# Optimization experiments

Measured on AMD Instinct MI355X. Metric: run time of the kernel, lower is better.

Reference implementation:

```python
import jax, jax.numpy as jnp
import numpy as np

SEQ_LEN, BATCH, INPUT, HID, LAYERS, TARGET_LEN = 120, 2048, 6, 64, 4, 120


def _cell(x_t, h, c, Wih, Whh, b):
    # torch LSTM gate order: input, forget, cell(g), output
    gates = x_t @ Wih.T + h @ Whh.T + b  # [B, 4H]
    i, f, g, o = jnp.split(gates, 4, axis=-1)
    c_new = jax.nn.sigmoid(f) * c + jax.nn.sigmoid(i) * jnp.tanh(g)
    h_new = jax.nn.sigmoid(o) * jnp.tanh(c_new)
    return h_new, c_new


def _stack_step(h, c, x_t, Wih0, Wih, Whh, b):
    # one time step through all stacked layers; h, c: [L, B, H]
    hs, cs = [], []
    inp = x_t
    L = Whh.shape[0]
    for l in range(L):
        W = Wih0 if l == 0 else Wih[l - 1]
        hn, cn = _cell(inp, h[l], c[l], W, Whh[l], b[l])
        hs.append(hn)
        cs.append(cn)
        inp = hn
    return jnp.stack(hs), jnp.stack(cs), inp


def setup_inputs() -> dict:
    key = jax.random.key(0)
    ks = jax.random.split(key, 11)
    s = 1.0 / np.sqrt(HID)  # torch LSTM uniform init scale
    u = lambda k, shp: jax.random.uniform(k, shp, jnp.float32, -s, s)
    return {
        "x": jax.random.normal(ks[0], (SEQ_LEN, BATCH, INPUT), jnp.float32),
        "enc_Wih0": u(ks[1], (4 * HID, INPUT)),
        "enc_Wih": u(ks[2], (LAYERS - 1, 4 * HID, HID)),
        "enc_Whh": u(ks[3], (LAYERS, 4 * HID, HID)),
        "enc_b": u(ks[4], (LAYERS, 4 * HID)),
        "dec_Wih0": u(ks[5], (4 * HID, INPUT)),
        "dec_Wih": u(ks[6], (LAYERS - 1, 4 * HID, HID)),
        "dec_Whh": u(ks[7], (LAYERS, 4 * HID, HID)),
        "dec_b": u(ks[8], (LAYERS, 4 * HID)),
        "lin_W": u(ks[9], (INPUT, HID)),
        "lin_b": u(ks[10], (INPUT,)),
        "target_len": TARGET_LEN,
    }


def reference(x, enc_Wih0, enc_Wih, enc_Whh, enc_b,
              dec_Wih0, dec_Wih, dec_Whh, dec_b, lin_W, lin_b, target_len):
    L, B, H = enc_Whh.shape[0], x.shape[1], enc_Whh.shape[-1]
    h0 = jnp.zeros((L, B, H), x.dtype)

    # ---- encoder: stacked LSTM over the input sequence (zero init state) ----
    def enc_step(carry, x_t):
        h, c = carry
        h, c, _ = _stack_step(h, c, x_t, enc_Wih0, enc_Wih, enc_Whh, enc_b)
        return (h, c), None

    (h, c), _ = jax.lax.scan(enc_step, (h0, h0), x)

    # ---- decoder: recursive one-step decode for target_len steps ----
    def dec_step(carry, _):
        h, c, inp = carry
        h, c, top = _stack_step(h, c, inp, dec_Wih0, dec_Wih, dec_Whh, dec_b)
        out = top @ lin_W.T + lin_b  # [B, INPUT]
        return (h, c, out), out

    last_in = x[-1]  # decoder seeded with last observed frame
    _, outputs = jax.lax.scan(dec_step, (h, c, last_in), None, length=target_len)
    return outputs  # [target_len, B, INPUT]
```

## Files before the change

kernel.cpp:

```cpp
#include <hip/hip_runtime.h>


#define S_LEN 120
#define BATCH 2048
#define NIN   6
#define H     64
#define NL    4
#define TLEN  120

#define HPAD 72

#define FRAGS_HALF 60
#define PACK_H8    (2 * FRAGS_HALF * 4 * 64)
#define PROJ_H8    (2 * 64)
#define NPACK      ((PACK_H8 + PROJ_H8) * 8)
#define EPACK_EL   (256 * 64 * 8)
#define NTOT       (NPACK + EPACK_EL)

#define WS_HOFF (768 * 1024)
#define WS_COFF (WS_HOFF + 1024 * 1024)

#define PERM(kk) ((((kk) & 3) << 4) | ((kk) >> 2))
#define PI(c)    ((((c) & 15) << 2) | ((c) >> 4))

#define SNEG (-1.44269504088896341f)
#define SGG  ( 2.88539008177792681f)
#define GGCLAMP 57.7078016355585362f
#define C2L2E 2.88539008177792681f

typedef _Float16 h8    __attribute__((ext_vector_type(8)));
typedef _Float16 hh2   __attribute__((ext_vector_type(2)));
typedef float    f32x4 __attribute__((ext_vector_type(4)));

__device__ __forceinline__ void bar_lgkm() {
  asm volatile("s_waitcnt lgkmcnt(0)\n\ts_barrier" ::: "memory");
}

__device__ __forceinline__ float swz16(float v) {
  int i = __builtin_bit_cast(int, v);
  i = __builtin_amdgcn_ds_swizzle(i, 0x401F);
  return __builtin_bit_cast(float, i);
}

__device__ __forceinline__ float ex2(float x) {
#if __has_builtin(__builtin_amdgcn_exp2f)
  return __builtin_amdgcn_exp2f(x);
#else
  return __expf(x * 0.693147180559945309f);
#endif
}

__global__ void prep_weights(const float* __restrict__ eWih0,
                             const float* __restrict__ eWih,
                             const float* __restrict__ eWhh,
                             const float* __restrict__ dWih0,
                             const float* __restrict__ dWih,
                             const float* __restrict__ dWhh,
                             const float* __restrict__ linW,
                             _Float16* __restrict__ wq) {
  int idx = blockIdx.x * blockDim.x + threadIdx.x;
  if (idx >= NTOT) return;

  if (idx >= NPACK) {
    int p    = idx - NPACK;
    int j    = p & 7;
    int lane = (p >> 3) & 63;
    int fe   = p >> 9;
    int kt   = fe & 3, nt = (fe >> 2) & 15, l = fe >> 6;
    int g    = nt * 16 + (lane & 15);
    int koff = ((lane >> 4) << 3) + j;
    float v = 0.0f;
    if (l == 0) {
      if (kt == 0)      v = (koff < NIN) ? eWih0[g * NIN + koff] : 0.0f;
      else if (kt == 1) v = 0.0f;
      else { int kk = (kt - 2) * 32 + koff; v = eWhh[g * H + PERM(kk)]; }
    } else {
      if (kt < 2) { int kk = kt * 32 + koff;
                    v = eWih[((l - 1) * 256 + g) * H + PERM(kk)]; }
      else        { int kk = (kt - 2) * 32 + koff;
                    v = eWhh[(l * 256 + g) * H + PERM(kk)]; }
    }
    v *= ((nt >> 2) == 2) ? SGG : SNEG;
    wq[idx] = (_Float16)v;
    return;
  }

  if (idx >= PACK_H8 * 8) {
    int p    = idx - PACK_H8 * 8;
    int j    = p & 7;
    int lane = (p >> 3) & 63;
    int fr   = p >> 9;
    int m    = lane & 15;
    int k    = fr * 32 + ((lane >> 4) << 3) + j;
    wq[idx] = (_Float16)((m < NIN) ? linW[m * H + k] : 0.0f);
    return;
  }

  const int j    = idx & 7;
  const int lane = (idx >> 3) & 63;
  const int wv   = (idx >> 9) & 3;
  const int fh   = idx >> 11;
  const int f    = fh % FRAGS_HALF;
  const int half = fh / FRAGS_HALF;
  const float* Wi0 = half ? dWih0 : eWih0;
  const float* Wi  = half ? dWih  : eWih;
  const float* Wh  = half ? dWhh  : eWhh;
  int l, q, kt;
  if (f < 12) { l = 0; q = f / 3; kt = f % 3; }
  else        { int ff = f - 12; l = 1 + ff / 16; ff %= 16; q = ff / 4; kt = ff % 4; }
  const int g    = q * 64 + wv * 16 + (lane & 15);
  const int k_in = ((lane >> 4) << 3) + j;
  float v;
  if (l == 0) {
    if (kt == 0) v = (k_in < NIN) ? Wi0[g * NIN + k_in] : 0.0f;
    else         v = Wh[g * H + (kt - 1) * 32 + k_in];
  } else {
    if (kt < 2) v = Wi[((l - 1) * 256 + g) * H + kt * 32 + k_in];
    else        v = Wh[(l * 256 + g) * H + (kt - 2) * 32 + k_in];
  }
  v *= (q == 2) ? SGG : SNEG;
  wq[idx] = (_Float16)v;
}

__device__ __forceinline__ float rcpf(float x) { return __builtin_amdgcn_rcpf(x); }
__device__ __forceinline__ f32x4 mf(h8 a, h8 b, f32x4 c) {
  return __builtin_amdgcn_mfma_f32_16x16x32_f16(a, b, c, 0, 0, 0);
}
#define SPLAT(v) ((f32x4){(v), (v), (v), (v)})

__device__ __forceinline__ float ew_one(float gi, float gf, float gg, float go,
                                        float& c) {
  gg = fminf(fmaxf(gg, -GGCLAMP), GGCLAMP);
  float eni = ex2(gi);
  float e2g = ex2(gg);
  float enf = ex2(gf);
  float eno = ex2(go);
  c = c * rcpf(1.0f + enf) + (e2g - 1.0f) * rcpf((1.0f + eni) * (e2g + 1.0f));
  float cc = fminf(fmaxf(c, -20.0f), 20.0f);
  float e2c = ex2(cc * C2L2E);
  return (e2c - 1.0f) * rcpf((1.0f + eno) * (e2c + 1.0f));
}

__device__ __forceinline__ void cell_ew(f32x4 g0, f32x4 g1, f32x4 g2, f32x4 g3,
                                        f32x4& c, _Float16* outbuf,
                                        int quad, int r16, int sl) {
  #pragma unroll
  for (int r = 0; r < 4; r++) {
    float cv = c[r];
    float hv = ew_one(g0[r], g1[r], g2[r], g3[r], cv);
    c[r] = cv;
    outbuf[(quad * 4 + r) * HPAD + sl * 16 + r16] = (_Float16)hv;
  }
}

__device__ __forceinline__ void precc(const h8 (&w)[8], h8 ar0, h8 ar1,
                                      f32x4 b, f32x4 (&ac)[4]) {
  #pragma unroll
  for (int q = 0; q < 4; q++)
    ac[q] = mf(ar1, w[q * 2 + 1], mf(ar0, w[q * 2], SPLAT(b[q])));
}
__device__ __forceinline__ void fireHc(const h8 (&w)[8], h8 ai0, h8 ai1,
                                       const f32x4 (&ac)[4], f32x4& c,
                                       _Float16* outbuf, int quad, int r16, int sl) {
  f32x4 g0 = mf(ai1, w[1], mf(ai0, w[0], ac[0]));
  f32x4 g1 = mf(ai1, w[3], mf(ai0, w[2], ac[1]));
  f32x4 g2 = mf(ai1, w[5], mf(ai0, w[4], ac[2]));
  f32x4 g3 = mf(ai1, w[7], mf(ai0, w[6], ac[3]));
  cell_ew(g0, g1, g2, g3, c, outbuf, quad, r16, sl);
}
__device__ __forceinline__ void fire0c(const h8 (&w)[4], h8 ax,
                                       const f32x4 (&ac)[4], f32x4& c,
                                       _Float16* outbuf, int quad, int r16, int sl) {
  f32x4 g0 = mf(ax, w[0], ac[0]);
  f32x4 g1 = mf(ax, w[1], ac[1]);
  f32x4 g2 = mf(ax, w[2], ac[2]);
  f32x4 g3 = mf(ax, w[3], ac[3]);
  cell_ew(g0, g1, g2, g3, c, outbuf, quad, r16, sl);
}
__device__ __forceinline__ void readA(const _Float16* buf, int r16, int quad,
                                      h8& a0, h8& a1) {
  a0 = *(const h8*)(buf + r16 * HPAD + quad * 8);
  a1 = *(const h8*)(buf + r16 * HPAD + 32 + quad * 8);
}

__global__ void __launch_bounds__(512, 2)
lstm_enc(const float* __restrict__ X,
         const float* __restrict__ encb,
         const h8* __restrict__ WQ,
         _Float16* __restrict__ hG,
         float* __restrict__ cG) {
  __shared__ _Float16 Hb[NL][2][16][HPAD];
  __shared__ _Float16 Xb[2][16][HPAD];

  const int tid  = threadIdx.x;
  const int wv   = tid >> 6;
  const int lane = tid & 63;
  const int quad = lane >> 4;
  const int r16  = lane & 15;
  const int grp  = wv & 1;
  const int lw   = (wv >> 1) & 3;
  const int bbase = blockIdx.x * 16;

  {
    float* p = (float*)&Hb[0][0][0][0];
    for (int i = tid; i < 4608; i += 512) p[i] = 0.0f;
    float* px = (float*)&Xb[0][0][0];
    for (int i = tid; i < 1152; i += 512) px[i] = 0.0f;
  }
  if (tid < 16 * NIN) {
    int m = tid / NIN, ii = tid - m * NIN;
    Xb[0][m][ii] = (_Float16)X[((size_t)0 * BATCH + bbase + m) * NIN + ii];
  }

  h8 we[8][4];
  #pragma unroll
  for (int q = 0; q < 4; q++)
    #pragma unroll
    for (int cc = 0; cc < 2; cc++)
      #pragma unroll
      for (int kt = 0; kt < 4; kt++)
        we[q * 2 + cc][kt] =
            WQ[(PACK_H8 + PROJ_H8) +
               ((lw * 64 + (q * 4 + 2 * grp + cc) * 4 + kt) * 64 + lane)];
  float ben[8];
  #pragma unroll
  for (int q = 0; q < 4; q++)
    #pragma unroll
    for (int cc = 0; cc < 2; cc++)
      ben[q * 2 + cc] = encb[lw * 256 + q * 64 + (2 * grp + cc) * 16 + r16] *
                        ((q == 2) ? SGG : SNEG);

  f32x4 ce[2];
  ce[0] = SPLAT(0.f); ce[1] = SPLAT(0.f);

  const bool pfLane = (wv == 0) && (lane < 48);
  const int  pe0 = lane * 2, pe1 = pe0 + 1;
  const int  pm0 = pe0 / NIN, pc0 = pe0 % NIN;
  const int  pm1 = pe1 / NIN, pc1 = pe1 % NIN;
  float pf0 = 0.f, pf1 = 0.f;
  if (pfLane) {
    const float* xs = X + ((size_t)1 * BATCH + bbase) * NIN;
    pf0 = xs[pe0]; pf1 = xs[pe1];
  }

  __syncthreads();

  #pragma unroll 1
  for (int i = 0; i < S_LEN + NL - 1; i++) {
    const int p = i & 1;
    const bool active = (i >= lw) && (i - lw < S_LEN);
    if (active) {
      const _Float16* inb = (lw == 0) ? &Xb[p][0][0] : &Hb[lw - 1][p ^ 1][0][0];
      const _Float16* rcb = &Hb[lw][p ^ 1][0][0];
      h8 ai0 = *(const h8*)(inb + r16 * HPAD + quad * 8);
      h8 ai1 = {};
      if (lw) ai1 = *(const h8*)(inb + r16 * HPAD + 32 + quad * 8);
      h8 ar0 = *(const h8*)(rcb + r16 * HPAD + quad * 8);
      h8 ar1 = *(const h8*)(rcb + r16 * HPAD + 32 + quad * 8);

      float nf0 = 0.f, nf1 = 0.f;
      if (pfLane && (i + 2 < S_LEN)) {
        const float* xs = X + ((size_t)(i + 2) * BATCH + bbase) * NIN;
        nf0 = xs[pe0]; nf1 = xs[pe1];
      }

      f32x4 a[8];
      #pragma unroll
      for (int j = 0; j < 8; j++) {
        f32x4 t = SPLAT(ben[j]);
        t = mf(ai0, we[j][0], t);
        if (lw) t = mf(ai1, we[j][1], t);
        t = mf(ar0, we[j][2], t);
        t = mf(ar1, we[j][3], t);
        a[j] = t;
      }

      _Float16* wb = &Hb[lw][p][0][0];
      #pragma unroll
      for (int r = 0; r < 4; r++) {
        hh2 hv;
        #pragma unroll
        for (int cc = 0; cc < 2; cc++) {
          float cv = ce[cc][r];
          hv[cc] = (_Float16)ew_one(a[cc][r], a[2 + cc][r],
                                    a[4 + cc][r], a[6 + cc][r], cv);
          ce[cc][r] = cv;
        }
        *(hh2*)(wb + (quad * 4 + r) * HPAD + 4 * r16 + 2 * grp) = hv;
      }

      if (pfLane && (i + 1 < S_LEN)) {
        Xb[p ^ 1][pm0][pc0] = (_Float16)pf0;
        Xb[p ^ 1][pm1][pc1] = (_Float16)pf1;
      }
      pf0 = nf0; pf1 = nf1;
    }
    bar_lgkm();
  }

  #pragma unroll
  for (int cc = 0; cc < 2; cc++)
    #pragma unroll
    for (int r = 0; r < 4; r++)
      cG[((size_t)lw * BATCH + bbase + quad * 4 + r) * H +
         (2 * grp + cc) * 16 + r16] = ce[cc][r];

  #pragma unroll
  for (int u = 0; u < 8; u++) {
    int i2 = tid + u * 512;
    int c = i2 & 63, m = (i2 >> 6) & 15, l = (i2 >> 10) & 3;
    hG[((size_t)l * BATCH + bbase + m) * H + c] =
        Hb[l][(l + 1) & 1][m][PI(c)];
  }
}

__global__ void __launch_bounds__(512, 2)
lstm_dec(const float* __restrict__ X,
         const float* __restrict__ decb,
         const float* __restrict__ linb,
         const h8* __restrict__ WQ,
         const _Float16* __restrict__ hG,
         const float* __restrict__ cG,
         float* __restrict__ out) {
  __shared__ _Float16 Hb[NL][2][16][HPAD];
  __shared__ f32x4 ACs[NL][4][4][64];

  const int tid   = threadIdx.x;
  const int wv    = tid >> 6;
  const int sl    = wv & 3;
  const int roleP = wv >> 2;
  const int lane  = tid & 63;
  const int quad  = lane >> 4;
  const int r16   = lane & 15;
  const int bbase = blockIdx.x * 16;

  #pragma unroll
  for (int u = 0; u < 8; u++) {
    int i2 = tid + u * 512;
    int l = i2 >> 10, m = (i2 >> 6) & 15, c = i2 & 63;
    Hb[l][1][m][c] = hG[((size_t)l * BATCH + bbase + m) * H + c];
  }
  __syncthreads();

  if (roleP) {
    h8 wp0[8], wpH[3][8];
    #pragma unroll
    for (int e = 0; e < 8; e++) {
      int q = e >> 1, k = e & 1;
      wp0[e] = WQ[((FRAGS_HALF + q * 3 + 1 + k) * 4 + sl) * 64 + lane];
    }
    #pragma unroll
    for (int l = 0; l < 3; l++)
      #pragma unroll
      for (int e = 0; e < 8; e++) {
        int q = e >> 1, k = e & 1;
        wpH[l][e] = WQ[((FRAGS_HALF + 12 + l * 16 + q * 4 + 2 + k) * 4 + sl) * 64 + lane];
      }
    f32x4 b0, b1, b2, b3;
    #pragma unroll
    for (int q = 0; q < 4; q++) {
      const float s = (q == 2) ? SGG : SNEG;
      b0[q] = decb[0 * 256 + q * 64 + sl * 16 + r16] * s;
      b1[q] = decb[1 * 256 + q * 64 + sl * 16 + r16] * s;
      b2[q] = decb[2 * 256 + q * 64 + sl * 16 + r16] * s;
      b3[q] = decb[3 * 256 + q * 64 + sl * 16 + r16] * s;
    }

    {
      h8 s0, s1;
      f32x4 a[4];
      readA(&Hb[0][1][0][0], r16, quad, s0, s1);
      precc(wp0, s0, s1, b0, a);
      #pragma unroll
      for (int j = 0; j < 4; j++) ACs[0][sl][j][lane] = a[j];
      readA(&Hb[1][1][0][0], r16, quad, s0, s1);
      precc(wpH[0], s0, s1, b1, a);
      #pragma unroll
      for (int j = 0; j < 4; j++) ACs[1][sl][j][lane] = a[j];
      readA(&Hb[2][1][0][0], r16, quad, s0, s1);
      precc(wpH[1], s0, s1, b2, a);
      #pragma unroll
      for (int j = 0; j < 4; j++) ACs[2][sl][j][lane] = a[j];
    }
    bar_lgkm();

    #pragma unroll 1
    for (int t = 0; t < TLEN; t++) {
      const int cur = t & 1, prv = cur ^ 1;
      {
        h8 a0, a1; readA(&Hb[3][prv][0][0], r16, quad, a0, a1);
        f32x4 a[4]; precc(wpH[2], a0, a1, b3, a);
        #pragma unroll
        for (int j = 0; j < 4; j++) ACs[3][sl][j][lane] = a[j];
        bar_lgkm();
      }
      {
        h8 a0, a1; readA(&Hb[0][cur][0][0], r16, quad, a0, a1);
        f32x4 a[4]; precc(wp0, a0, a1, b0, a);
        #pragma unroll
        for (int j = 0; j < 4; j++) ACs[0][sl][j][lane] = a[j];
        bar_lgkm();
      }
      {
        h8 a0, a1; readA(&Hb[1][cur][0][0], r16, quad, a0, a1);
        f32x4 a[4]; precc(wpH[0], a0, a1, b1, a);
        #pragma unroll
        for (int j = 0; j < 4; j++) ACs[1][sl][j][lane] = a[j];
        bar_lgkm();
      }
      {
        h8 a0, a1; readA(&Hb[2][cur][0][0], r16, quad, a0, a1);
        f32x4 a[4]; precc(wpH[1], a0, a1, b2, a);
        #pragma unroll
        for (int j = 0; j < 4; j++) ACs[2][sl][j][lane] = a[j];
        bar_lgkm();
      }
    }
  } else {
    h8 wf0[4], wfH[3][8];
    #pragma unroll
    for (int q = 0; q < 4; q++)
      wf0[q] = WQ[((FRAGS_HALF + q * 3) * 4 + sl) * 64 + lane];
    #pragma unroll
    for (int l = 0; l < 3; l++)
      #pragma unroll
      for (int e = 0; e < 8; e++) {
        int q = e >> 1, k = e & 1;
        wfH[l][e] = WQ[((FRAGS_HALF + 12 + l * 16 + q * 4 + k) * 4 + sl) * 64 + lane];
      }

    f32x4 cs0, cs1, cs2, cs3;
    #pragma unroll
    for (int r = 0; r < 4; r++) {
      cs0[r] = cG[((size_t)0 * BATCH + bbase + quad * 4 + r) * H + sl * 16 + r16];
      cs1[r] = cG[((size_t)1 * BATCH + bbase + quad * 4 + r) * H + sl * 16 + r16];
      cs2[r] = cG[((size_t)2 * BATCH + bbase + quad * 4 + r) * H + sl * 16 + r16];
      cs3[r] = cG[((size_t)3 * BATCH + bbase + quad * 4 + r) * H + sl * 16 + r16];
    }

    h8 lwA0 = WQ[PACK_H8 + lane];
    h8 lwA1 = WQ[PACK_H8 + 64 + lane];
    f32x4 lbq;
    #pragma unroll
    for (int r = 0; r < 4; r++)
      lbq[r] = (quad * 4 + r < NIN) ? linb[quad * 4 + r] : 0.0f;

    h8 xseed = {};
    if (quad == 0) {
      const float* xs = X + ((size_t)(S_LEN - 1) * BATCH + bbase + r16) * NIN;
      #pragma unroll
      for (int j = 0; j < 6; j++) xseed[j] = (_Float16)xs[j];
    }

    bar_lgkm();

    __builtin_amdgcn_s_setprio(1);

    #pragma unroll 1
    for (int t = 0; t < TLEN; t++) {
      const int cur = t & 1, prv = cur ^ 1;
      {
        h8 ar0, ar1;
        readA(&Hb[3][prv][0][0], r16, quad, ar0, ar1);
        h8 ax;
        if (t == 0) {
          ax = xseed;
        } else {
          f32x4 ap = lbq;
          ap = mf(lwA0, ar0, ap);
          ap = mf(lwA1, ar1, ap);
          if (sl == 0) {
            #pragma unroll
            for (int r = 0; r < 4; r++) {
              const int fm = quad * 4 + r;
              if (fm < NIN)
                out[((size_t)(t - 1) * BATCH + bbase + r16) * NIN + fm] = ap[r];
            }
          }
          float x4 = swz16(ap[0]);
          float x5 = swz16(ap[1]);
          h8 xa = {};
          xa[0] = (_Float16)ap[0]; xa[1] = (_Float16)ap[1];
          xa[2] = (_Float16)ap[2]; xa[3] = (_Float16)ap[3];
          xa[4] = (_Float16)x4;    xa[5] = (_Float16)x5;
          h8 zz = {};
          ax = (quad == 0) ? xa : zz;
        }
        f32x4 ac[4];
        #pragma unroll
        for (int j = 0; j < 4; j++) ac[j] = ACs[0][sl][j][lane];
        fire0c(wf0, ax, ac, cs0, &Hb[0][cur][0][0], quad, r16, sl);
        bar_lgkm();
      }
      {
        h8 ai0, ai1;
        readA(&Hb[0][cur][0][0], r16, quad, ai0, ai1);
        f32x4 ac[4];
        #pragma unroll
        for (int j = 0; j < 4; j++) ac[j] = ACs[1][sl][j][lane];
        fireHc(wfH[0], ai0, ai1, ac, cs1, &Hb[1][cur][0][0], quad, r16, sl);
        bar_lgkm();
      }
      {
        h8 ai0, ai1;
        readA(&Hb[1][cur][0][0], r16, quad, ai0, ai1);
        f32x4 ac[4];
        #pragma unroll
        for (int j = 0; j < 4; j++) ac[j] = ACs[2][sl][j][lane];
        fireHc(wfH[1], ai0, ai1, ac, cs2, &Hb[2][cur][0][0], quad, r16, sl);
        bar_lgkm();
      }
      {
        h8 ai0, ai1;
        readA(&Hb[2][cur][0][0], r16, quad, ai0, ai1);
        f32x4 ac[4];
        #pragma unroll
        for (int j = 0; j < 4; j++) ac[j] = ACs[3][sl][j][lane];
        fireHc(wfH[2], ai0, ai1, ac, cs3, &Hb[3][cur][0][0], quad, r16, sl);
        bar_lgkm();
      }
    }

    __builtin_amdgcn_s_setprio(0);

    if (sl == 0) {
      h8 ar0, ar1;
      readA(&Hb[3][1][0][0], r16, quad, ar0, ar1);
      f32x4 ap = lbq;
      ap = mf(lwA0, ar0, ap);
      ap = mf(lwA1, ar1, ap);
      #pragma unroll
      for (int r = 0; r < 4; r++) {
        const int fm = quad * 4 + r;
        if (fm < NIN)
          out[((size_t)(TLEN - 1) * BATCH + bbase + r16) * NIN + fm] = ap[r];
      }
    }
  }
}

extern "C" void kernel_launch(void* const* d_in, const int* in_sizes, int n_in,
                              void* d_out, int out_size, void* d_ws, size_t ws_size,
                              hipStream_t stream) {
  const float* X     = (const float*)d_in[0];
  const float* eWih0 = (const float*)d_in[1];
  const float* eWih  = (const float*)d_in[2];
  const float* eWhh  = (const float*)d_in[3];
  const float* eb    = (const float*)d_in[4];
  const float* dWih0 = (const float*)d_in[5];
  const float* dWih  = (const float*)d_in[6];
  const float* dWhh  = (const float*)d_in[7];
  const float* db    = (const float*)d_in[8];
  const float* lW    = (const float*)d_in[9];
  const float* lb    = (const float*)d_in[10];

  _Float16* wq = (_Float16*)d_ws;
  _Float16* hG = (_Float16*)((char*)d_ws + WS_HOFF);
  float*    cG = (float*)((char*)d_ws + WS_COFF);

  prep_weights<<<(NTOT + 255) / 256, 256, 0, stream>>>(
      eWih0, eWih, eWhh, dWih0, dWih, dWhh, lW, wq);

  lstm_enc<<<BATCH / 16, 512, 0, stream>>>(
      X, eb, (const h8*)wq, hG, cG);

  lstm_dec<<<BATCH / 16, 512, 0, stream>>>(
      X, db, lb, (const h8*)wq, hG, cG, (float*)d_out);
}
```

Before: 489.0 us.

## Split decoder cell elementwise work between projection and fire wave groups

The decoder's precompute waves (roleP) now also compute the input-side MFMAs and the gate nonlinearities for rows 2-3 of each quad. The fire waves handle only rows 0-1, which halves the serial elementwise tail on the critical path. The precompute waves re-read their fire weights from global memory every step, because keeping them in registers would exceed the budget; an opaque offset stops the compiler from hoisting those loads. The cost is extra global/L2 traffic and more MFMAs on the precompute waves, which could become the new bottleneck at the barriers.

```diff
diff --git a/kernel.cpp b/kernel.cpp
--- a/kernel.cpp
+++ b/kernel.cpp
@@ -31,6 +31,7 @@
 typedef _Float16 h8    __attribute__((ext_vector_type(8)));
 typedef _Float16 hh2   __attribute__((ext_vector_type(2)));
 typedef float    f32x4 __attribute__((ext_vector_type(4)));
+typedef float    f32x2 __attribute__((ext_vector_type(2)));
 
 __device__ __forceinline__ void bar_lgkm() {
   asm volatile("s_waitcnt lgkmcnt(0)\n\ts_barrier" ::: "memory");
@@ -153,29 +154,25 @@
   }
 }
 
+__device__ __forceinline__ void ew_pair(const f32x4& g0, const f32x4& g1,
+                                        const f32x4& g2, const f32x4& g3,
+                                        f32x2& c, _Float16* outbuf,
+                                        int quad, int r16, int sl, int rb) {
+  float cv0 = c[0];
+  float h0 = ew_one(g0[rb], g1[rb], g2[rb], g3[rb], cv0);
+  c[0] = cv0;
+  outbuf[(quad * 4 + rb) * HPAD + sl * 16 + r16] = (_Float16)h0;
+  float cv1 = c[1];
+  float h1 = ew_one(g0[rb + 1], g1[rb + 1], g2[rb + 1], g3[rb + 1], cv1);
+  c[1] = cv1;
+  outbuf[(quad * 4 + rb + 1) * HPAD + sl * 16 + r16] = (_Float16)h1;
+}
+
 __device__ __forceinline__ void precc(const h8 (&w)[8], h8 ar0, h8 ar1,
                                       f32x4 b, f32x4 (&ac)[4]) {
   #pragma unroll
   for (int q = 0; q < 4; q++)
     ac[q] = mf(ar1, w[q * 2 + 1], mf(ar0, w[q * 2], SPLAT(b[q])));
-}
-__device__ __forceinline__ void fireHc(const h8 (&w)[8], h8 ai0, h8 ai1,
-                                       const f32x4 (&ac)[4], f32x4& c,
-                                       _Float16* outbuf, int quad, int r16, int sl) {
-  f32x4 g0 = mf(ai1, w[1], mf(ai0, w[0], ac[0]));
-  f32x4 g1 = mf(ai1, w[3], mf(ai0, w[2], ac[1]));
-  f32x4 g2 = mf(ai1, w[5], mf(ai0, w[4], ac[2]));
-  f32x4 g3 = mf(ai1, w[7], mf(ai0, w[6], ac[3]));
-  cell_ew(g0, g1, g2, g3, c, outbuf, quad, r16, sl);
-}
-__device__ __forceinline__ void fire0c(const h8 (&w)[4], h8 ax,
-                                       const f32x4 (&ac)[4], f32x4& c,
-                                       _Float16* outbuf, int quad, int r16, int sl) {
-  f32x4 g0 = mf(ax, w[0], ac[0]);
-  f32x4 g1 = mf(ax, w[1], ac[1]);
-  f32x4 g2 = mf(ax, w[2], ac[2]);
-  f32x4 g3 = mf(ax, w[3], ac[3]);
-  cell_ew(g0, g1, g2, g3, c, outbuf, quad, r16, sl);
 }
 __device__ __forceinline__ void readA(const _Float16* buf, int r16, int quad,
                                       h8& a0, h8& a1) {
@@ -342,6 +339,19 @@
   }
   __syncthreads();
 
+  h8 xseed = {};
+  if (quad == 0) {
+    const float* xs = X + ((size_t)(S_LEN - 1) * BATCH + bbase + r16) * NIN;
+    #pragma unroll
+    for (int j = 0; j < 6; j++) xseed[j] = (_Float16)xs[j];
+  }
+  h8 lwA0 = WQ[PACK_H8 + lane];
+  h8 lwA1 = WQ[PACK_H8 + 64 + lane];
+  f32x4 lbq;
+  #pragma unroll
+  for (int r = 0; r < 4; r++)
+    lbq[r] = (quad * 4 + r < NIN) ? linb[quad * 4 + r] : 0.0f;
+
   if (roleP) {
     h8 wp0[8], wpH[3][8];
     #pragma unroll
@@ -365,6 +375,14 @@
       b2[q] = decb[2 * 256 + q * 64 + sl * 16 + r16] * s;
       b3[q] = decb[3 * 256 + q * 64 + sl * 16 + r16] * s;
     }
+    f32x2 cp0, cp1, cp2, cp3;
+    #pragma unroll
+    for (int j = 0; j < 2; j++) {
+      cp0[j] = cG[((size_t)0 * BATCH + bbase + quad * 4 + 2 + j) * H + sl * 16 + r16];
+      cp1[j] = cG[((size_t)1 * BATCH + bbase + quad * 4 + 2 + j) * H + sl * 16 + r16];
+      cp2[j] = cG[((size_t)2 * BATCH + bbase + quad * 4 + 2 + j) * H + sl * 16 + r16];
+      cp3[j] = cG[((size_t)3 * BATCH + bbase + quad * 4 + 2 + j) * H + sl * 16 + r16];
+    }
 
     {
       h8 s0, s1;
@@ -389,30 +407,98 @@
       const int cur = t & 1, prv = cur ^ 1;
       {
         h8 a0, a1; readA(&Hb[3][prv][0][0], r16, quad, a0, a1);
+        int ofs = 0; asm volatile("" : "+v"(ofs));
+        h8 t0 = WQ[ofs + ((FRAGS_HALF + 0) * 4 + sl) * 64 + lane];
+        h8 t1 = WQ[ofs + ((FRAGS_HALF + 3) * 4 + sl) * 64 + lane];
+        h8 t2 = WQ[ofs + ((FRAGS_HALF + 6) * 4 + sl) * 64 + lane];
+        h8 t3 = WQ[ofs + ((FRAGS_HALF + 9) * 4 + sl) * 64 + lane];
         f32x4 a[4]; precc(wpH[2], a0, a1, b3, a);
         #pragma unroll
         for (int j = 0; j < 4; j++) ACs[3][sl][j][lane] = a[j];
+        h8 ax;
+        if (t == 0) {
+          ax = xseed;
+        } else {
+          f32x4 ap = lbq;
+          ap = mf(lwA0, a0, ap);
+          ap = mf(lwA1, a1, ap);
+          float x4 = swz16(ap[0]);
+          float x5 = swz16(ap[1]);
+          h8 xa = {};
+          xa[0] = (_Float16)ap[0]; xa[1] = (_Float16)ap[1];
+          xa[2] = (_Float16)ap[2]; xa[3] = (_Float16)ap[3];
+          xa[4] = (_Float16)x4;    xa[5] = (_Float16)x5;
+          h8 zz = {};
+          ax = (quad == 0) ? xa : zz;
+        }
+        f32x4 g0 = mf(ax, t0, ACs[0][sl][0][lane]);
+        f32x4 g1 = mf(ax, t1, ACs[0][sl][1][lane]);
+        f32x4 g2 = mf(ax, t2, ACs[0][sl][2][lane]);
+        f32x4 g3 = mf(ax, t3, ACs[0][sl][3][lane]);
+        ew_pair(g0, g1, g2, g3, cp0, &Hb[0][cur][0][0], quad, r16, sl, 2);
         bar_lgkm();
       }
       {
         h8 a0, a1; readA(&Hb[0][cur][0][0], r16, quad, a0, a1);
+        int ofs = 0; asm volatile("" : "+v"(ofs));
+        h8 t0 = WQ[ofs + ((FRAGS_HALF + 12 + 0) * 4 + sl) * 64 + lane];
+        h8 t1 = WQ[ofs + ((FRAGS_HALF + 12 + 1) * 4 + sl) * 64 + lane];
+        h8 t2 = WQ[ofs + ((FRAGS_HALF + 12 + 4) * 4 + sl) * 64 + lane];
+        h8 t3 = WQ[ofs + ((FRAGS_HALF + 12 + 5) * 4 + sl) * 64 + lane];
+        h8 t4 = WQ[ofs + ((FRAGS_HALF + 12 + 8) * 4 + sl) * 64 + lane];
+        h8 t5 = WQ[ofs + ((FRAGS_HALF + 12 + 9) * 4 + sl) * 64 + lane];
+        h8 t6 = WQ[ofs + ((FRAGS_HALF + 12 + 12) * 4 + sl) * 64 + lane];
+        h8 t7 = WQ[ofs + ((FRAGS_HALF + 12 + 13) * 4 + sl) * 64 + lane];
         f32x4 a[4]; precc(wp0, a0, a1, b0, a);
         #pragma unroll
         for (int j = 0; j < 4; j++) ACs[0][sl][j][lane] = a[j];
+        f32x4 g0 = mf(a1, t1, mf(a0, t0, ACs[1][sl][0][lane]));
+        f32x4 g1 = mf(a1, t3, mf(a0, t2, ACs[1][sl][1][lane]));
+        f32x4 g2 = mf(a1, t5, mf(a0, t4, ACs[1][sl][2][lane]));
+        f32x4 g3 = mf(a1, t7, mf(a0, t6, ACs[1][sl][3][lane]));
+        ew_pair(g0, g1, g2, g3, cp1, &Hb[1][cur][0][0], quad, r16, sl, 2);
         bar_lgkm();
       }
       {
         h8 a0, a1; readA(&Hb[1][cur][0][0], r16, quad, a0, a1);
+        int ofs = 0; asm volatile("" : "+v"(ofs));
+        h8 t0 = WQ[ofs + ((FRAGS_HALF + 12 + 16 + 0) * 4 + sl) * 64 + lane];
+        h8 t1 = WQ[ofs + ((FRAGS_HALF + 12 + 16 + 1) * 4 + sl) * 64 + lane];
+        h8 t2 = WQ[ofs + ((FRAGS_HALF + 12 + 16 + 4) * 4 + sl) * 64 + lane];
+        h8 t3 = WQ[ofs + ((FRAGS_HALF + 12 + 16 + 5) * 4 + sl) * 64 + lane];
+        h8 t4 = WQ[ofs + ((FRAGS_HALF + 12 + 16 + 8) * 4 + sl) * 64 + lane];
+        h8 t5 = WQ[ofs + ((FRAGS_HALF + 12 + 16 + 9) * 4 + sl) * 64 + lane];
+        h8 t6 = WQ[ofs + ((FRAGS_HALF + 12 + 16 + 12) * 4 + sl) * 64 + lane];
+        h8 t7 = WQ[ofs + ((FRAGS_HALF + 12 + 16 + 13) * 4 + sl) * 64 + lane];
         f32x4 a[4]; precc(wpH[0], a0, a1, b1, a);
         #pragma unroll
         for (int j = 0; j < 4; j++) ACs[1][sl][j][lane] = a[j];
+        f32x4 g0 = mf(a1, t1, mf(a0, t0, ACs[2][sl][0][lane]));
+        f32x4 g1 = mf(a1, t3, mf(a0, t2, ACs[2][sl][1][lane]));
+        f32x4 g2 = mf(a1, t5, mf(a0, t4, ACs[2][sl][2][lane]));
+        f32x4 g3 = mf(a1, t7, mf(a0, t6, ACs[2][sl][3][lane]));
+        ew_pair(g0, g1, g2, g3, cp2, &Hb[2][cur][0][0], quad, r16, sl, 2);
         bar_lgkm();
       }
       {
         h8 a0, a1; readA(&Hb[2][cur][0][0], r16, quad, a0, a1);
+        int ofs = 0; asm volatile("" : "+v"(ofs));
+        h8 t0 = WQ[ofs + ((FRAGS_HALF + 12 + 32 + 0) * 4 + sl) * 64 + lane];
+        h8 t1 = WQ[ofs + ((FRAGS_HALF + 12 + 32 + 1) * 4 + sl) * 64 + lane];
+        h8 t2 = WQ[ofs + ((FRAGS_HALF + 12 + 32 + 4) * 4 + sl) * 64 + lane];
+        h8 t3 = WQ[ofs + ((FRAGS_HALF + 12 + 32 + 5) * 4 + sl) * 64 + lane];
+        h8 t4 = WQ[ofs + ((FRAGS_HALF + 12 + 32 + 8) * 4 + sl) * 64 + lane];
+        h8 t5 = WQ[ofs + ((FRAGS_HALF + 12 + 32 + 9) * 4 + sl) * 64 + lane];
+        h8 t6 = WQ[ofs + ((FRAGS_HALF + 12 + 32 + 12) * 4 + sl) * 64 + lane];
+        h8 t7 = WQ[ofs + ((FRAGS_HALF + 12 + 32 + 13) * 4 + sl) * 64 + lane];
         f32x4 a[4]; precc(wpH[1], a0, a1, b2, a);
         #pragma unroll
         for (int j = 0; j < 4; j++) ACs[2][sl][j][lane] = a[j];
+        f32x4 g0 = mf(a1, t1, mf(a0, t0, ACs[3][sl][0][lane]));
+        f32x4 g1 = mf(a1, t3, mf(a0, t2, ACs[3][sl][1][lane]));
+        f32x4 g2 = mf(a1, t5, mf(a0, t4, ACs[3][sl][2][lane]));
+        f32x4 g3 = mf(a1, t7, mf(a0, t6, ACs[3][sl][3][lane]));
+        ew_pair(g0, g1, g2, g3, cp3, &Hb[3][cur][0][0], quad, r16, sl, 2);
         bar_lgkm();
       }
     }
@@ -429,27 +515,13 @@
         wfH[l][e] = WQ[((FRAGS_HALF + 12 + l * 16 + q * 4 + k) * 4 + sl) * 64 + lane];
       }
 
-    f32x4 cs0, cs1, cs2, cs3;
-    #pragma unroll
-    for (int r = 0; r < 4; r++) {
-      cs0[r] = cG[((size_t)0 * BATCH + bbase + quad * 4 + r) * H + sl * 16 + r16];
-      cs1[r] = cG[((size_t)1 * BATCH + bbase + quad * 4 + r) * H + sl * 16 + r16];
-      cs2[r] = cG[((size_t)2 * BATCH + bbase + quad * 4 + r) * H + sl * 16 + r16];
-      cs3[r] = cG[((size_t)3 * BATCH + bbase + quad * 4 + r) * H + sl * 16 + r16];
-    }
-
-    h8 lwA0 = WQ[PACK_H8 + lane];
-    h8 lwA1 = WQ[PACK_H8 + 64 + lane];
-    f32x4 lbq;
-    #pragma unroll
-    for (int r = 0; r < 4; r++)
-      lbq[r] = (quad * 4 + r < NIN) ? linb[quad * 4 + r] : 0.0f;
-
-    h8 xseed = {};
-    if (quad == 0) {
-      const float* xs = X + ((size_t)(S_LEN - 1) * BATCH + bbase + r16) * NIN;
-      #pragma unroll
-      for (int j = 0; j < 6; j++) xseed[j] = (_Float16)xs[j];
+    f32x2 cf0, cf1, cf2, cf3;
+    #pragma unroll
+    for (int j = 0; j < 2; j++) {
+      cf0[j] = cG[((size_t)0 * BATCH + bbase + quad * 4 + j) * H + sl * 16 + r16];
+      cf1[j] = cG[((size_t)1 * BATCH + bbase + quad * 4 + j) * H + sl * 16 + r16];
+      cf2[j] = cG[((size_t)2 * BATCH + bbase + quad * 4 + j) * H + sl * 16 + r16];
+      cf3[j] = cG[((size_t)3 * BATCH + bbase + quad * 4 + j) * H + sl * 16 + r16];
     }
 
     bar_lgkm();
@@ -486,37 +558,41 @@
           h8 zz = {};
           ax = (quad == 0) ? xa : zz;
         }
-        f32x4 ac[4];
-        #pragma unroll
-        for (int j = 0; j < 4; j++) ac[j] = ACs[0][sl][j][lane];
-        fire0c(wf0, ax, ac, cs0, &Hb[0][cur][0][0], quad, r16, sl);
+        f32x4 g0 = mf(ax, wf0[0], ACs[0][sl][0][lane]);
+        f32x4 g1 = mf(ax, wf0[1], ACs[0][sl][1][lane]);
+        f32x4 g2 = mf(ax, wf0[2], ACs[0][sl][2][lane]);
+        f32x4 g3 = mf(ax, wf0[3], ACs[0][sl][3][lane]);
+        ew_pair(g0, g1, g2, g3, cf0, &Hb[0][cur][0][0], quad, r16, sl, 0);
         bar_lgkm();
       }
       {
         h8 ai0, ai1;
         readA(&Hb[0][cur][0][0], r16, quad, ai0, ai1);
-        f32x4 ac[4];
-        #pragma unroll
-        for (int j = 0; j < 4; j++) ac[j] = ACs[1][sl][j][lane];
-        fireHc(wfH[0], ai0, ai1, ac, cs1, &Hb[1][cur][0][0], quad, r16, sl);
+        f32x4 g0 = mf(ai1, wfH[0][1], mf(ai0, wfH[0][0], ACs[1][sl][0][lane]));
+        f32x4 g1 = mf(ai1, wfH[0][3], mf(ai0, wfH[0][2], ACs[1][sl][1][lane]));
+        f32x4 g2 = mf(ai1, wfH[0][5], mf(ai0, wfH[0][4], ACs[1][sl][2][lane]));
+        f32x4 g3 = mf(ai1, wfH[0][7], mf(ai0, wfH[0][6], ACs[1][sl][3][lane]));
+        ew_pair(g0, g1, g2, g3, cf1, &Hb[1][cur][0][0], quad, r16, sl, 0);
         bar_lgkm();
       }
       {
         h8 ai0, ai1;
         readA(&Hb[1][cur][0][0], r16, quad, ai0, ai1);
-        f32x4 ac[4];
-        #pragma unroll
-        for (int j = 0; j < 4; j++) ac[j] = ACs[2][sl][j][lane];
-        fireHc(wfH[1], ai0, ai1, ac, cs2, &Hb[2][cur][0][0], quad, r16, sl);
+        f32x4 g0 = mf(ai1, wfH[1][1], mf(ai0, wfH[1][0], ACs[2][sl][0][lane]));
+        f32x4 g1 = mf(ai1, wfH[1][3], mf(ai0, wfH[1][2], ACs[2][sl][1][lane]));
+        f32x4 g2 = mf(ai1, wfH[1][5], mf(ai0, wfH[1][4], ACs[2][sl][2][lane]));
+        f32x4 g3 = mf(ai1, wfH[1][7], mf(ai0, wfH[1][6], ACs[2][sl][3][lane]));
+        ew_pair(g0, g1, g2, g3, cf2, &Hb[2][cur][0][0], quad, r16, sl, 0);
         bar_lgkm();
       }
       {
         h8 ai0, ai1;
         readA(&Hb[2][cur][0][0], r16, quad, ai0, ai1);
-        f32x4 ac[4];
-        #pragma unroll
-        for (int j = 0; j < 4; j++) ac[j] = ACs[3][sl][j][lane];
-        fireHc(wfH[2], ai0, ai1, ac, cs3, &Hb[3][cur][0][0], quad, r16, sl);
+        f32x4 g0 = mf(ai1, wfH[2][1], mf(ai0, wfH[2][0], ACs[3][sl][0][lane]));
+        f32x4 g1 = mf(ai1, wfH[2][3], mf(ai0, wfH[2][2], ACs[3][sl][1][lane]));
+        f32x4 g2 = mf(ai1, wfH[2][5], mf(ai0, wfH[2][4], ACs[3][sl][2][lane]));
+        f32x4 g3 = mf(ai1, wfH[2][7], mf(ai0, wfH[2][6], ACs[3][sl][3][lane]));
+        ew_pair(g0, g1, g2, g3, cf3, &Hb[3][cur][0][0], quad, r16, sl, 0);
         bar_lgkm();
       }
     }
```

After: 794.6 us. +62.5%, slower.
